# Kernel tuning notes

Measured on AMD Instinct MI355X. Metric: run time of the kernel, lower is better.

## Reference

```python
import jax, jax.numpy as jnp
import numpy as np
from jax import lax

B, K, D = 8, 256, 256
T_FRAMES = 2048
NH, HD = 4, 64          # num_heads_upsampling = 2*num_heads, head_dim = in_dim // NH
FW = FC = 8             # filter_size_w / filter_size_c
SW, SC = 16, 2          # swish_block_units


def setup_inputs() -> dict:
    key = jax.random.key(0)
    ks = jax.random.split(key, 24)
    rn = lambda i, shape, s=0.05: jax.random.normal(ks[i], shape, jnp.float32) * s
    return {
        'phs': rn(0, (B, K, D), 1.0),
        'phs_mask': jnp.ones((B, K), bool),
        'total_duration_groundtruth': jnp.full((B,), T_FRAMES, jnp.int32),
        'T': T_FRAMES,
        'Wd': rn(1, (D, 1)), 'bd': jnp.zeros((1,), jnp.float32),
        'W1': rn(2, (D, D)), 'b1': jnp.zeros((D,), jnp.float32),
        'W2': rn(3, (D, D)), 'b2': jnp.zeros((D,), jnp.float32),
        'W3': rn(4, (D, D)), 'b3': jnp.zeros((D,), jnp.float32),
        'wconv_k': rn(5, (FW, D, 3)), 'wconv_b': jnp.zeros((FW,), jnp.float32),
        'wln_g': jnp.ones((FW,), jnp.float32), 'wln_b': jnp.zeros((FW,), jnp.float32),
        'cconv_k': rn(6, (FC, D, 3)), 'cconv_b': jnp.zeros((FC,), jnp.float32),
        'cln_g': jnp.ones((FC,), jnp.float32), 'cln_b': jnp.zeros((FC,), jnp.float32),
        'sw1_W': rn(7, (FW + 2, SW)), 'sw1_b': jnp.zeros((SW,), jnp.float32),
        'sw2_W': rn(8, (SW, SW)), 'sw2_b': jnp.zeros((SW,), jnp.float32),
        'sc1_W': rn(9, (FC + 2, SC)), 'sc1_b': jnp.zeros((SC,), jnp.float32),
        'sc2_W': rn(10, (SC, SC)), 'sc2_b': jnp.zeros((SC,), jnp.float32),
        'we_W': rn(11, (SW, NH)), 'we_b': jnp.zeros((NH,), jnp.float32),
        'ce_W': rn(12, (SC, HD)), 'ce_b': jnp.zeros((HD,), jnp.float32),
    }


def _silu(x):
    return x * jax.nn.sigmoid(x)


def _conv_ln_silu(x, kern, bias, g, beta):
    # x: (b,k,D) -> Conv1d (same pad) -> LayerNorm over channel dim -> SiLU -> (b,k,F)
    y = lax.conv_general_dilated(x.transpose(0, 2, 1), kern, (1,), [(1, 1)],
                                 dimension_numbers=('NCH', 'OIH', 'NCH'))
    y = y + bias[None, :, None]
    mu = y.mean(1, keepdims=True)
    var = y.var(1, keepdims=True)
    y = (y - mu) * lax.rsqrt(var + 1e-5) * g[None, :, None] + beta[None, :, None]
    return _silu(y).transpose(0, 2, 1)


def _forward(phs, phs_mask, total_duration_groundtruth, t,
             Wd, bd, W1, b1, W2, b2, W3, b3,
             wconv_k, wconv_b, wln_g, wln_b, cconv_k, cconv_b, cln_g, cln_b,
             sw1_W, sw1_b, sw2_W, sw2_b, sc1_W, sc1_b, sc2_W, sc2_b,
             we_W, we_b, ce_W, ce_b):
    b, k, D = phs.shape
    nh, hd = NH, HD
    v_pad = ~phs_mask                                       # (b,k)
    # duration predictor (encoder substituted by identity; see notes)
    d_log = jax.nn.relu(phs @ Wd + bd)[..., 0]              # (b,k)
    d = jnp.clip(jnp.exp(d_log) - 1.0, 1e-12)
    d = jnp.where(v_pad, 0.0, d)
    d_pad = jnp.arange(t)[None, :] >= total_duration_groundtruth[:, None]  # (b,t)
    attn_mask = v_pad[:, None, :] | d_pad[:, :, None]       # (b,t,k)
    e = jnp.cumsum(d, -1)
    s = e - d
    scale = jnp.arange(1, t + 1, dtype=phs.dtype)[None, :, None]
    s_b = jnp.where(attn_mask, 0.0, scale - s[:, None, :])  # (b,t,k)
    e_b = jnp.where(attn_mask, 0.0, e[:, None, :] - scale)
    v = phs @ W1 + b1                                        # mha_project_1
    # w path: conv features broadcast over t + per-position MLP -> softmax scores
    w_convs = _conv_ln_silu(v, wconv_k, wconv_b, wln_g, wln_b)  # (b,k,FW)
    merged_w = jnp.concatenate([s_b[..., None], e_b[..., None],
                                jnp.broadcast_to(w_convs[:, None], (b, t, k, FW))], -1)
    hw = _silu(merged_w @ sw1_W + sw1_b)
    hw = _silu(hw @ sw2_W + sw2_b)                           # (b,t,k,SW)
    logits = (hw @ we_W + we_b).transpose(0, 3, 1, 2)        # (b,nh,t,k)
    logits = jnp.where(v_pad[:, None, None, :], -jnp.inf, logits)
    attn = jax.nn.softmax(logits, -1)                        # (b,nh,t,k)
    # c path
    c_convs = _conv_ln_silu(v, cconv_k, cconv_b, cln_g, cln_b)  # (b,k,FC)
    merged_c = jnp.concatenate([s_b[..., None], e_b[..., None],
                                jnp.broadcast_to(c_convs[:, None], (b, t, k, FC))], -1)
    hc = _silu(merged_c @ sc1_W + sc1_b)
    hc = _silu(hc @ sc2_W + sc2_b)                           # (b,t,k,SC)
    ein = jnp.einsum('bhtk,btkp->bhtp', attn, hc)            # (b,nh,t,SC)
    c_extra = (ein @ ce_W + ce_b).transpose(0, 2, 1, 3)      # (b,t,nh,hd)
    v4 = v.reshape(b, k, nh, hd).transpose(0, 2, 1, 3)       # (b,nh,k,hd)
    o_left = jnp.einsum('bhtk,bhkd->bhtd', attn, v4).transpose(0, 2, 1, 3)
    o_left = o_left.reshape(b, t, nh * hd) @ W2 + b2
    o_right = c_extra.reshape(b, t, nh * hd) @ W3 + b3
    out = o_left + o_right
    return out, d, attn


def reference(phs, phs_mask, total_duration_groundtruth, T,
              Wd, bd, W1, b1, W2, b2, W3, b3,
              wconv_k, wconv_b, wln_g, wln_b, cconv_k, cconv_b, cln_g, cln_b,
              sw1_W, sw1_b, sw2_W, sw2_b, sc1_W, sc1_b, sc2_W, sc2_b,
              we_W, we_b, ce_W, ce_b):
    return _forward(phs, phs_mask, total_duration_groundtruth, int(T),
                    Wd, bd, W1, b1, W2, b2, W3, b3,
                    wconv_k, wconv_b, wln_g, wln_b, cconv_k, cconv_b, cln_g, cln_b,
                    sw1_W, sw1_b, sw2_W, sw2_b, sc1_W, sc1_b, sc2_W, sc2_b,
                    we_W, we_b, ce_W, ce_b)
```

## Files before the change

kernel.cpp:

```cpp
#include <hip/hip_runtime.h>
#include <hip/hip_bf16.h>
#include <math.h>

#define BB 8
#define KK 256
#define DD 256
#define TT 2048
#define NH 4
#define HD 64
#define FW 8
#define FC 8
#define TPB 8
#define NK3 1088

#define OFF_S    0
#define OFF_E    (OFF_S + BB*KK)
#define OFF_V    (OFF_E + BB*KK)
#define OFF_WC   (OFF_V + BB*KK*DD)
#define OFF_CC   (OFF_WC + BB*KK*FW)
#define OFF_C0   (OFF_CC + BB*KK*FC)
#define OFF_W1T  (OFF_C0 + DD)
#define OFF_W2T  (OFF_W1T + DD*DD)
#define OFF_U2B  (OFF_W2T + DD*DD)
#define OFF_EINB (OFF_U2B + BB*DD*NK3/2)
#define OFF_P3   (OFF_EINB + BB*TT*64/2)

#define OUT_OUT  0
#define OUT_D    (BB*TT*DD)
#define OUT_ATTN (OUT_D + BB*KK)

typedef __attribute__((ext_vector_type(8))) short s8v;
typedef __attribute__((ext_vector_type(4))) float f4v;
typedef __attribute__((ext_vector_type(2))) _Float16 h2v;
typedef unsigned short ushort_t;

#define BC(x) __builtin_bit_cast(h2v, (unsigned int)(x))

__device__ __forceinline__ h2v pk(float a, float b) {
    return __builtin_bit_cast(h2v, __builtin_amdgcn_cvt_pkrtz(a, b));
}
__device__ __forceinline__ ushort_t f2bf(float x) {
    unsigned u = __float_as_uint(x);
    u += 0x7fffu + ((u >> 16) & 1u);
    return (ushort_t)(u >> 16);
}

#if __has_builtin(__builtin_amdgcn_fdot2)
#define FDOT2(a,b,c) __builtin_amdgcn_fdot2((a),(b),(c),false)
#else
__device__ __forceinline__ float FDOT2(h2v a, h2v b, float c) {
    return c + (float)a[0]*(float)b[0] + (float)a[1]*(float)b[1];
}
#endif

__device__ __forceinline__ float siluf(float z) {
    return z * __builtin_amdgcn_rcpf(1.0f + __expf(-z));
}

__device__ __forceinline__ float rsum64d(float x) {
    x += __int_as_float(__builtin_amdgcn_update_dpp(0, __float_as_int(x), 0x111, 0xf, 0xf, true));
    x += __int_as_float(__builtin_amdgcn_update_dpp(0, __float_as_int(x), 0x112, 0xf, 0xf, true));
    x += __int_as_float(__builtin_amdgcn_update_dpp(0, __float_as_int(x), 0x114, 0xf, 0xf, true));
    x += __int_as_float(__builtin_amdgcn_update_dpp(0, __float_as_int(x), 0x118, 0xf, 0xf, true));
    x += __int_as_float(__builtin_amdgcn_update_dpp(0, __float_as_int(x), 0x142, 0xa, 0xf, true));
    x += __int_as_float(__builtin_amdgcn_update_dpp(0, __float_as_int(x), 0x143, 0xc, 0xf, true));
    return x;
}
__device__ __forceinline__ float rmax64d(float x) {
    const int NI = 0xff800000;
    x = fmaxf(x, __int_as_float(__builtin_amdgcn_update_dpp(NI, __float_as_int(x), 0x111, 0xf, 0xf, false)));
    x = fmaxf(x, __int_as_float(__builtin_amdgcn_update_dpp(NI, __float_as_int(x), 0x112, 0xf, 0xf, false)));
    x = fmaxf(x, __int_as_float(__builtin_amdgcn_update_dpp(NI, __float_as_int(x), 0x114, 0xf, 0xf, false)));
    x = fmaxf(x, __int_as_float(__builtin_amdgcn_update_dpp(NI, __float_as_int(x), 0x118, 0xf, 0xf, false)));
    x = fmaxf(x, __int_as_float(__builtin_amdgcn_update_dpp(NI, __float_as_int(x), 0x142, 0xa, 0xf, false)));
    x = fmaxf(x, __int_as_float(__builtin_amdgcn_update_dpp(NI, __float_as_int(x), 0x143, 0xc, 0xf, false)));
    return x;
}
__device__ __forceinline__ float lane63f(float x) {
    return __int_as_float(__builtin_amdgcn_readlane(__float_as_int(x), 63));
}

__launch_bounds__(256)
__global__ void prep(const float* __restrict__ W1, const float* __restrict__ W2,
                     const float* __restrict__ phs, const float* __restrict__ Wd,
                     const float* __restrict__ bd,
                     const float* __restrict__ ceW, const float* __restrict__ ceb,
                     const float* __restrict__ W3, const float* __restrict__ b3,
                     const float* __restrict__ b2,
                     float* __restrict__ ws, float* __restrict__ dout) {
    __shared__ float tl[64][65];
    __shared__ float dbuf[KK];
    int role = blockIdx.x, tid = threadIdx.x;
    if (role < 32) {
        const float* src = (role < 16) ? W1 : W2;
        float* dst = ws + ((role < 16) ? OFF_W1T : OFF_W2T);
        int rr = role & 15;
        int r0 = (rr >> 2)*64, c0 = (rr & 3)*64;
        int rx = tid >> 4, col4 = (tid & 15)*4;
#pragma unroll
        for (int i = 0; i < 4; ++i) {
            int row = rx + i*16;
            float4 vld = *(const float4*)&src[(size_t)(r0+row)*256 + c0 + col4];
            tl[row][col4+0]=vld.x; tl[row][col4+1]=vld.y; tl[row][col4+2]=vld.z; tl[row][col4+3]=vld.w;
        }
        __syncthreads();
#pragma unroll
        for (int i = 0; i < 4; ++i) {
            int row = rx + i*16;
            float4 vst;
            vst.x = tl[col4+0][row]; vst.y = tl[col4+1][row];
            vst.z = tl[col4+2][row]; vst.w = tl[col4+3][row];
            *(float4*)&dst[(size_t)(c0+row)*256 + r0 + col4] = vst;
        }
    } else if (role < 40) {
        int b = role - 32;
        int wave = tid >> 6, lane = tid & 63;
        float4 w4 = ((const float4*)Wd)[lane];
        float bd0 = bd[0];
        for (int kk = 0; kk < 64; ++kk) {
            int k = wave*64 + kk;
            float4 p = ((const float4*)(phs + (size_t)(b*KK + k)*DD))[lane];
            float part = p.x*w4.x + p.y*w4.y + p.z*w4.z + p.w*w4.w;
            float tot = rsum64d(part);
            if (lane == 63) {
                float acc = tot + bd0;
                float dl = fmaxf(acc, 0.f);
                dbuf[k] = fmaxf(expf(dl) - 1.f, 1e-12f);
            }
        }
        __syncthreads();
        int k = tid;
        float dv = dbuf[k];
        for (int off = 1; off < KK; off <<= 1) {
            float t = (k >= off) ? dbuf[k-off] : 0.f;
            __syncthreads();
            dbuf[k] += t;
            __syncthreads();
        }
        float e = dbuf[k];
        dout[OUT_D + b*KK + k] = dv;
        ws[OFF_S + b*KK + k] = e - dv;
        ws[OFF_E + b*KK + k] = e;
    } else if (role < 48) {
        int b = role - 40, c = tid;
        float acc[8] = {0,0,0,0,0,0,0,0};
        float c0v = b3[c] + b2[c];
#pragma unroll 4
        for (int h = 0; h < NH; ++h) {
            for (int d = 0; d < HD; ++d) {
                float w3v = W3[(size_t)(h*HD + d)*DD + c];
                acc[h*2+0] = fmaf(ceW[d],      w3v, acc[h*2+0]);
                acc[h*2+1] = fmaf(ceW[HD + d], w3v, acc[h*2+1]);
                c0v        = fmaf(ceb[d],      w3v, c0v);
            }
        }
        ushort_t* rowp = (ushort_t*)(ws + OFF_U2B) + ((size_t)b*DD + c)*NK3 + 1024;
#pragma unroll
        for (int j = 0; j < 8; ++j) rowp[j] = f2bf(acc[j]);
#pragma unroll
        for (int j = 8; j < 64; ++j) rowp[j] = 0;
        if (b == 0) ws[OFF_C0 + c] = c0v;
    } else {
        uint4* ez = (uint4*)((ushort_t*)(ws + OFF_EINB));
        int base = (role - 48) * 2048 + tid;
#pragma unroll
        for (int i = 0; i < 8; ++i) {
            uint4 z; z.x = 0; z.y = 0; z.z = 0; z.w = 0;
            ez[base + i*256] = z;
        }
    }
}

__launch_bounds__(256)
__global__ void k3a(const float* __restrict__ vsrc, const float* __restrict__ wk,
                    const float* __restrict__ ck, float* __restrict__ part) {
    __shared__ float vt[KK][33];
    __shared__ float wl[32][3][8];
    int b = blockIdx.x, ch = blockIdx.y, ph = blockIdx.z;
    const float* kern = ph ? ck : wk;
    int tid = threadIdx.x, c0 = ch*32;
    for (int i = tid; i < 768; i += 256) {
        int f = i & 7;
        int cq = i >> 3; int q = cq % 3; int cc = cq / 3;
        wl[cc][q][f] = kern[(f*DD + c0 + cc)*3 + q];
    }
    {
        int cc = tid & 31, r8 = tid >> 5;
        for (int j = 0; j < 32; ++j) {
            int row = r8 + j*8;
            vt[row][cc] = vsrc[(size_t)(b*KK + row)*DD + c0 + cc];
        }
    }
    __syncthreads();
    int k = tid;
    float y[8] = {0.f,0.f,0.f,0.f,0.f,0.f,0.f,0.f};
    bool hm = (k > 0), hp = (k < KK-1);
    for (int cc = 0; cc < 32; ++cc) {
        float xm = hm ? vt[k-1][cc] : 0.f;
        float x0 = vt[k][cc];
        float xp = hp ? vt[k+1][cc] : 0.f;
        float4 a0 = *(const float4*)&wl[cc][0][0];
        float4 a1 = *(const float4*)&wl[cc][0][4];
        float4 b0 = *(const float4*)&wl[cc][1][0];
        float4 b1 = *(const float4*)&wl[cc][1][4];
        float4 c0v = *(const float4*)&wl[cc][2][0];
        float4 c1v = *(const float4*)&wl[cc][2][4];
        y[0] = fmaf(xm, a0.x, fmaf(x0, b0.x, fmaf(xp, c0v.x, y[0])));
        y[1] = fmaf(xm, a0.y, fmaf(x0, b0.y, fmaf(xp, c0v.y, y[1])));
        y[2] = fmaf(xm, a0.z, fmaf(x0, b0.z, fmaf(xp, c0v.z, y[2])));
        y[3] = fmaf(xm, a0.w, fmaf(x0, b0.w, fmaf(xp, c0v.w, y[3])));
        y[4] = fmaf(xm, a1.x, fmaf(x0, b1.x, fmaf(xp, c1v.x, y[4])));
        y[5] = fmaf(xm, a1.y, fmaf(x0, b1.y, fmaf(xp, c1v.y, y[5])));
        y[6] = fmaf(xm, a1.z, fmaf(x0, b1.z, fmaf(xp, c1v.z, y[6])));
        y[7] = fmaf(xm, a1.w, fmaf(x0, b1.w, fmaf(xp, c1v.w, y[7])));
    }
    float* pp = part + ((((size_t)(b*2 + ph))*8 + ch)*KK + k)*8;
    *(float4*)&pp[0] = make_float4(y[0],y[1],y[2],y[3]);
    *(float4*)&pp[4] = make_float4(y[4],y[5],y[6],y[7]);
}

__global__ void k3b(float* __restrict__ ws_, const float* __restrict__ part,
                    const float* __restrict__ wb, const float* __restrict__ wg, const float* __restrict__ wbe,
                    const float* __restrict__ cb, const float* __restrict__ cg, const float* __restrict__ cbe) {
    int b = blockIdx.x, k = threadIdx.x;
#pragma unroll
    for (int ph = 0; ph < 2; ++ph) {
        const float* bias = ph ? cb : wb;
        const float* g    = ph ? cg : wg;
        const float* beta = ph ? cbe : wbe;
        float y[8];
#pragma unroll
        for (int f = 0; f < 8; ++f) y[f] = bias[f];
        for (int ch = 0; ch < 8; ++ch) {
            const float* pp = part + ((((size_t)(b*2 + ph))*8 + ch)*KK + k)*8;
            float4 q0 = *(const float4*)&pp[0];
            float4 q1 = *(const float4*)&pp[4];
            y[0]+=q0.x; y[1]+=q0.y; y[2]+=q0.z; y[3]+=q0.w;
            y[4]+=q1.x; y[5]+=q1.y; y[6]+=q1.z; y[7]+=q1.w;
        }
        float mu = 0.f;
#pragma unroll
        for (int f = 0; f < 8; ++f) mu += y[f];
        mu *= 0.125f;
        float var = 0.f;
#pragma unroll
        for (int f = 0; f < 8; ++f) { float dd = y[f]-mu; var = fmaf(dd, dd, var); }
        var *= 0.125f;
        float inv = rsqrtf(var + 1e-5f);
        float* dst = ws_ + (ph ? OFF_CC : OFF_WC) + (size_t)(b*KK + k)*8;
#pragma unroll
        for (int f = 0; f < 8; ++f) {
            float z = (y[f]-mu)*inv*g[f] + beta[f];
            dst[f] = siluf(z);
        }
    }
}

__launch_bounds__(256, 3)
__global__ void k4_main(const float* __restrict__ ws, const int* __restrict__ tdur,
                        const float* __restrict__ sw1W, const float* __restrict__ sw1b,
                        const float* __restrict__ sw2W, const float* __restrict__ sw2b,
                        const float* __restrict__ weW, const float* __restrict__ web,
                        const float* __restrict__ sc1W, const float* __restrict__ sc1b,
                        const float* __restrict__ sc2W, const float* __restrict__ sc2b,
                        float* __restrict__ dout, ushort_t* __restrict__ einb) {
    __shared__ float sw1s[160];
    __shared__ float sw1bs[16];
    __shared__ float sc1s[20];
    __shared__ float sc1bs[2];
    __shared__ h2v   sw2h[16][8];
    __shared__ float sw2bias[16];
    __shared__ float wes4[16][4];
    __shared__ float webs[4], sc2s[4], sc2bs[2];
    __shared__ float red[4][4][16];
    __shared__ float gbuf[4][4][4];
    int tid = threadIdx.x;
    int b = blockIdx.y;
    int t0 = blockIdx.x * TPB;
    int lane = tid & 63, wid = tid >> 6;

    if (tid < 160) sw1s[tid] = sw1W[tid];
    if (tid < 16)  { sw1bs[tid] = sw1b[tid]; sw2bias[tid] = sw2b[tid]; }
    if (tid < 20)  sc1s[tid] = sc1W[tid];
    if (tid < 2)   { sc1bs[tid] = sc1b[tid]; sc2bs[tid] = sc2b[tid]; }
    if (tid < 4)   { webs[tid] = web[tid]; sc2s[tid] = sc2W[tid]; }
    if (tid < 128) {
        int j = tid >> 3, ip = tid & 7;
        sw2h[j][ip] = pk(sw2W[(2*ip)*16 + j], sw2W[(2*ip+1)*16 + j]);
    }
    if (tid < 64) wes4[tid>>2][tid&3] = weW[tid];
    __syncthreads();

    int k = tid;
    float s_k = ws[OFF_S + b*KK + k];
    float e_k = ws[OFF_E + b*KK + k];
    float al[16], be[16];
    float lgm[4], p2m[2];
    {
        float wcf[8];
        const float* wp = ws + OFF_WC + (size_t)(b*KK + k)*8;
#pragma unroll
        for (int f = 0; f < 8; ++f) wcf[f] = wp[f];
        float bw[16];
#pragma unroll
        for (int j = 0; j < 16; ++j) {
            float z = sw1bs[j];
#pragma unroll
            for (int f = 0; f < 8; ++f) z = fmaf(wcf[f], sw1s[(2+f)*16 + j], z);
            bw[j] = z;
        }
        h2v h1pm[8];
#pragma unroll
        for (int ip = 0; ip < 8; ++ip)
            h1pm[ip] = pk(siluf(bw[2*ip]), siluf(bw[2*ip+1]));
        lgm[0]=webs[0]; lgm[1]=webs[1]; lgm[2]=webs[2]; lgm[3]=webs[3];
#pragma unroll
        for (int j = 0; j < 16; ++j) {
            const uint4* wpq = (const uint4*)&sw2h[j][0];
            uint4 wa = wpq[0], wb = wpq[1];
            float z = sw2bias[j];
            z = FDOT2(h1pm[0], BC(wa.x), z); z = FDOT2(h1pm[1], BC(wa.y), z);
            z = FDOT2(h1pm[2], BC(wa.z), z); z = FDOT2(h1pm[3], BC(wa.w), z);
            z = FDOT2(h1pm[4], BC(wb.x), z); z = FDOT2(h1pm[5], BC(wb.y), z);
            z = FDOT2(h1pm[6], BC(wb.z), z); z = FDOT2(h1pm[7], BC(wb.w), z);
            float g = siluf(z);
            float4 wv = *(const float4*)&wes4[j][0];
            lgm[0] = fmaf(g, wv.x, lgm[0]); lgm[1] = fmaf(g, wv.y, lgm[1]);
            lgm[2] = fmaf(g, wv.z, lgm[2]); lgm[3] = fmaf(g, wv.w, lgm[3]);
        }
#pragma unroll
        for (int j = 0; j < 16; ++j) {
            float wsj = sw1s[j], wej = sw1s[16 + j];
            be[j] = wsj - wej;
            al[j] = bw[j] - wsj*s_k + wej*e_k;
        }
    }
    float gc[2], dc[2];
    {
        float ccf[8];
        const float* cp = ws + OFF_CC + (size_t)(b*KK + k)*8;
#pragma unroll
        for (int f = 0; f < 8; ++f) ccf[f] = cp[f];
        float bc0 = sc1bs[0], bc1 = sc1bs[1];
#pragma unroll
        for (int f = 0; f < 8; ++f) {
            bc0 = fmaf(ccf[f], sc1s[(2+f)*2 + 0], bc0);
            bc1 = fmaf(ccf[f], sc1s[(2+f)*2 + 1], bc1);
        }
        gc[0] = sc1s[0] - sc1s[2]; gc[1] = sc1s[1] - sc1s[3];
        dc[0] = bc0 - sc1s[0]*s_k + sc1s[2]*e_k;
        dc[1] = bc1 - sc1s[1]*s_k + sc1s[3]*e_k;
        float p1m0 = siluf(bc0), p1m1 = siluf(bc1);
        p2m[0] = siluf(p1m0*sc2s[0] + p1m1*sc2s[2] + sc2bs[0]);
        p2m[1] = siluf(p1m0*sc2s[1] + p1m1*sc2s[3] + sc2bs[1]);
    }
    float sc2r0 = sc2s[0], sc2r1 = sc2s[1], sc2r2 = sc2s[2], sc2r3 = sc2s[3];
    float sc2b0 = sc2bs[0], sc2b1 = sc2bs[1];
    float web0 = webs[0], web1 = webs[1], web2 = webs[2], web3 = webs[3];
    int td = tdur[b];

    for (int tg = 0; tg < TPB; tg += 4) {
        int tbase = t0 + tg;
        h2v h1p[4][8];
        float p2v[4][2];
        float lg[4][4];
        float ex[4][4];
#pragma unroll
        for (int u = 0; u < 4; ++u) {
            float tp1 = (float)(tbase + u + 1);
#pragma unroll
            for (int ip = 0; ip < 8; ++ip) {
                float z0 = siluf(fmaf(tp1, be[2*ip], al[2*ip]));
                float z1 = siluf(fmaf(tp1, be[2*ip+1], al[2*ip+1]));
                h1p[u][ip] = pk(z0, z1);
            }
            float p10 = siluf(fmaf(tp1, gc[0], dc[0]));
            float p11 = siluf(fmaf(tp1, gc[1], dc[1]));
            p2v[u][0] = siluf(p10*sc2r0 + p11*sc2r2 + sc2b0);
            p2v[u][1] = siluf(p10*sc2r1 + p11*sc2r3 + sc2b1);
            lg[u][0]=web0; lg[u][1]=web1; lg[u][2]=web2; lg[u][3]=web3;
        }
#pragma unroll
        for (int j = 0; j < 16; ++j) {
            const uint4* wpq = (const uint4*)&sw2h[j][0];
            uint4 wa = wpq[0], wb = wpq[1];
            h2v w0=BC(wa.x), w1=BC(wa.y), w2=BC(wa.z), w3=BC(wa.w);
            h2v w4_=BC(wb.x), w5=BC(wb.y), w6=BC(wb.z), w7=BC(wb.w);
            float bias = sw2bias[j];
            float4 wv = *(const float4*)&wes4[j][0];
#pragma unroll
            for (int u = 0; u < 4; ++u) {
                float z = bias;
                z = FDOT2(h1p[u][0], w0, z); z = FDOT2(h1p[u][1], w1, z);
                z = FDOT2(h1p[u][2], w2, z); z = FDOT2(h1p[u][3], w3, z);
                z = FDOT2(h1p[u][4], w4_, z); z = FDOT2(h1p[u][5], w5, z);
                z = FDOT2(h1p[u][6], w6, z); z = FDOT2(h1p[u][7], w7, z);
                float g = siluf(z);
                lg[u][0] = fmaf(g, wv.x, lg[u][0]);
                lg[u][1] = fmaf(g, wv.y, lg[u][1]);
                lg[u][2] = fmaf(g, wv.z, lg[u][2]);
                lg[u][3] = fmaf(g, wv.w, lg[u][3]);
            }
        }
#pragma unroll
        for (int u = 0; u < 4; ++u) {
            if ((tbase + u) >= td) {
                lg[u][0]=lgm[0]; lg[u][1]=lgm[1]; lg[u][2]=lgm[2]; lg[u][3]=lgm[3];
                p2v[u][0]=p2m[0]; p2v[u][1]=p2m[1];
            }
        }
#pragma unroll
        for (int u = 0; u < 4; ++u) {
            float m0 = lane63f(rmax64d(lg[u][0]));
            float m1 = lane63f(rmax64d(lg[u][1]));
            float m2 = lane63f(rmax64d(lg[u][2]));
            float m3 = lane63f(rmax64d(lg[u][3]));
            ex[u][0] = __expf(lg[u][0] - m0);
            ex[u][1] = __expf(lg[u][1] - m1);
            ex[u][2] = __expf(lg[u][2] - m2);
            ex[u][3] = __expf(lg[u][3] - m3);
            float s0 = rsum64d(ex[u][0]), s1 = rsum64d(ex[u][1]);
            float s2 = rsum64d(ex[u][2]), s3 = rsum64d(ex[u][3]);
            float u0 = rsum64d(ex[u][0]*p2v[u][0]);
            float u1 = rsum64d(ex[u][0]*p2v[u][1]);
            float u2 = rsum64d(ex[u][1]*p2v[u][0]);
            float u3 = rsum64d(ex[u][1]*p2v[u][1]);
            float u4 = rsum64d(ex[u][2]*p2v[u][0]);
            float u5 = rsum64d(ex[u][2]*p2v[u][1]);
            float u6 = rsum64d(ex[u][3]*p2v[u][0]);
            float u7 = rsum64d(ex[u][3]*p2v[u][1]);
            if (lane == 63) {
                float* rr = &red[u][wid][0];
                *(float4*)&rr[0]  = make_float4(m0, m1, m2, m3);
                *(float4*)&rr[4]  = make_float4(s0, s1, s2, s3);
                *(float4*)&rr[8]  = make_float4(u0, u1, u2, u3);
                *(float4*)&rr[12] = make_float4(u4, u5, u6, u7);
            }
        }
        __syncthreads();
        if (tid < 64) {
            int u = tid >> 4, h = (tid >> 2) & 3, w = tid & 3;
            float m0 = red[u][0][h], m1 = red[u][1][h], m2 = red[u][2][h], m3 = red[u][3][h];
            float M = fmaxf(fmaxf(m0, m1), fmaxf(m2, m3));
            float f0 = __expf(m0 - M), f1 = __expf(m1 - M);
            float f2 = __expf(m2 - M), f3 = __expf(m3 - M);
            float S = red[u][0][4+h]*f0 + red[u][1][4+h]*f1
                    + red[u][2][4+h]*f2 + red[u][3][4+h]*f3;
            float fw = (w == 0) ? f0 : ((w == 1) ? f1 : ((w == 2) ? f2 : f3));
            gbuf[u][w][h] = fw * __builtin_amdgcn_rcpf(S);
        } else if (tid < 96) {
            int idx = tid - 64, u = idx >> 3, j = idx & 7, h = j >> 1;
            float m0 = red[u][0][h], m1 = red[u][1][h], m2 = red[u][2][h], m3 = red[u][3][h];
            float M = fmaxf(fmaxf(m0, m1), fmaxf(m2, m3));
            float f0 = __expf(m0 - M), f1 = __expf(m1 - M);
            float f2 = __expf(m2 - M), f3 = __expf(m3 - M);
            float S = red[u][0][4+h]*f0 + red[u][1][4+h]*f1
                    + red[u][2][4+h]*f2 + red[u][3][4+h]*f3;
            float num = red[u][0][8+j]*f0 + red[u][1][8+j]*f1
                      + red[u][2][8+j]*f2 + red[u][3][8+j]*f3;
            einb[((size_t)b*TT + tbase + u)*64 + j] = f2bf(num * __builtin_amdgcn_rcpf(S));
        }
        __syncthreads();
#pragma unroll
        for (int u = 0; u < 4; ++u) {
            int t = tbase + u;
            float4 g4 = *(const float4*)&gbuf[u][wid][0];
            dout[OUT_ATTN + ((size_t)(b*NH + 0)*TT + t)*KK + k] = ex[u][0] * g4.x;
            dout[OUT_ATTN + ((size_t)(b*NH + 1)*TT + t)*KK + k] = ex[u][1] * g4.y;
            dout[OUT_ATTN + ((size_t)(b*NH + 2)*TT + t)*KK + k] = ex[u][2] * g4.z;
            dout[OUT_ATTN + ((size_t)(b*NH + 3)*TT + t)*KK + k] = ex[u][3] * g4.w;
        }
    }
}

#define MLDA 56
__launch_bounds__(256, 2)
__global__ void kmm(const float* __restrict__ A, const float* __restrict__ B,
                    float* __restrict__ C, const float* __restrict__ bias,
                    int Kd, int lda, int ldb, int ldc) {
    int m0 = blockIdx.x * 128, n0 = blockIdx.y * 128;
    __shared__ ushort_t Asl[128*MLDA];
    __shared__ ushort_t Bsl[128*MLDA];
    int tid = threadIdx.x;
    int lane = tid & 63, wid = tid >> 6;
    int wm = wid & 1, wn = wid >> 1;
    int quad = lane >> 4, lo = lane & 15;
    f4v acc[4][4];
#pragma unroll
    for (int i = 0; i < 4; ++i)
#pragma unroll
        for (int j = 0; j < 4; ++j) { f4v zz = {0.f,0.f,0.f,0.f}; acc[i][j] = zz; }
    int srow = tid >> 3;
    int scol = (tid & 7) * 4;
    for (int k0 = 0; k0 < Kd; k0 += 32) {
#pragma unroll
        for (int i = 0; i < 4; ++i) {
            int r = srow + i*32;
            float4 va = *(const float4*)&A[(size_t)(m0 + r)*lda + k0 + scol];
            float4 vb = *(const float4*)&B[(size_t)(n0 + r)*ldb + k0 + scol];
            __hip_bfloat162 pa0 = __float22bfloat162_rn(make_float2(va.x, va.y));
            __hip_bfloat162 pa1 = __float22bfloat162_rn(make_float2(va.z, va.w));
            __hip_bfloat162 pb0 = __float22bfloat162_rn(make_float2(vb.x, vb.y));
            __hip_bfloat162 pb1 = __float22bfloat162_rn(make_float2(vb.z, vb.w));
            *(uint2*)&Asl[r*MLDA + scol] = make_uint2(*(unsigned int*)&pa0, *(unsigned int*)&pa1);
            *(uint2*)&Bsl[r*MLDA + scol] = make_uint2(*(unsigned int*)&pb0, *(unsigned int*)&pb1);
        }
        __syncthreads();
        s8v af[4], bf[4];
#pragma unroll
        for (int mt = 0; mt < 4; ++mt)
            af[mt] = *(const s8v*)&Asl[(wm*64 + mt*16 + lo)*MLDA + quad*8];
#pragma unroll
        for (int nt = 0; nt < 4; ++nt)
            bf[nt] = *(const s8v*)&Bsl[(wn*64 + nt*16 + lo)*MLDA + quad*8];
#pragma unroll
        for (int mt = 0; mt < 4; ++mt)
#pragma unroll
            for (int nt = 0; nt < 4; ++nt)
                acc[mt][nt] = __builtin_amdgcn_mfma_f32_16x16x32_bf16(af[mt], bf[nt], acc[mt][nt], 0, 0, 0);
        __syncthreads();
    }
#pragma unroll
    for (int mt = 0; mt < 4; ++mt)
#pragma unroll
        for (int nt = 0; nt < 4; ++nt) {
            int col = n0 + wn*64 + nt*16 + lo;
            float bv = bias ? bias[col] : 0.f;
#pragma unroll
            for (int r = 0; r < 4; ++r) {
                int row = m0 + wm*64 + mt*16 + quad*4 + r;
                C[(size_t)row*ldc + col] = acc[mt][nt][r] + bv;
            }
        }
}

__launch_bounds__(256, 2)
__global__ void kmmB(const float* __restrict__ A, const float* __restrict__ B,
                     ushort_t* __restrict__ C,
                     int Kd, int lda, int ldb, int ldc,
                     long sA2, long sB1, long sB2, long sC1, long sC2, int nz2) {
    int z = blockIdx.z, z1 = z / nz2, z2 = z - z1*nz2;
    A += (size_t)z2*sA2;
    B += (size_t)z1*sB1 + (size_t)z2*sB2;
    C += (size_t)z1*sC1 + (size_t)z2*sC2;
    int m0 = blockIdx.x * 128, n0 = blockIdx.y * 128;
    __shared__ ushort_t Asl[128*MLDA];
    __shared__ ushort_t Bsl[128*MLDA];
    int tid = threadIdx.x;
    int lane = tid & 63, wid = tid >> 6;
    int wm = wid & 1, wn = wid >> 1;
    int quad = lane >> 4, lo = lane & 15;
    f4v acc[4][4];
#pragma unroll
    for (int i = 0; i < 4; ++i)
#pragma unroll
        for (int j = 0; j < 4; ++j) { f4v zz = {0.f,0.f,0.f,0.f}; acc[i][j] = zz; }
    int srow = tid >> 3;
    int scol = (tid & 7) * 4;
    for (int k0 = 0; k0 < Kd; k0 += 32) {
#pragma unroll
        for (int i = 0; i < 4; ++i) {
            int r = srow + i*32;
            float4 va = *(const float4*)&A[(size_t)(m0 + r)*lda + k0 + scol];
            float4 vb = *(const float4*)&B[(size_t)(n0 + r)*ldb + k0 + scol];
            __hip_bfloat162 pa0 = __float22bfloat162_rn(make_float2(va.x, va.y));
            __hip_bfloat162 pa1 = __float22bfloat162_rn(make_float2(va.z, va.w));
            __hip_bfloat162 pb0 = __float22bfloat162_rn(make_float2(vb.x, vb.y));
            __hip_bfloat162 pb1 = __float22bfloat162_rn(make_float2(vb.z, vb.w));
            *(uint2*)&Asl[r*MLDA + scol] = make_uint2(*(unsigned int*)&pa0, *(unsigned int*)&pa1);
            *(uint2*)&Bsl[r*MLDA + scol] = make_uint2(*(unsigned int*)&pb0, *(unsigned int*)&pb1);
        }
        __syncthreads();
        s8v af[4], bf[4];
#pragma unroll
        for (int mt = 0; mt < 4; ++mt)
            af[mt] = *(const s8v*)&Asl[(wm*64 + mt*16 + lo)*MLDA + quad*8];
#pragma unroll
        for (int nt = 0; nt < 4; ++nt)
            bf[nt] = *(const s8v*)&Bsl[(wn*64 + nt*16 + lo)*MLDA + quad*8];
#pragma unroll
        for (int mt = 0; mt < 4; ++mt)
#pragma unroll
            for (int nt = 0; nt < 4; ++nt)
                acc[mt][nt] = __builtin_amdgcn_mfma_f32_16x16x32_bf16(af[mt], bf[nt], acc[mt][nt], 0, 0, 0);
        __syncthreads();
    }
#pragma unroll
    for (int mt = 0; mt < 4; ++mt)
#pragma unroll
        for (int nt = 0; nt < 4; ++nt) {
            int col = n0 + wn*64 + nt*16 + lo;
#pragma unroll
            for (int r = 0; r < 4; ++r) {
                int row = m0 + wm*64 + mt*16 + quad*4 + r;
                C[(size_t)row*ldc + col] = f2bf(acc[mt][nt][r]);
            }
        }
}

#define OLD 72
__launch_bounds__(256, 4)
__global__ void kOL3(const float* __restrict__ attn, const ushort_t* __restrict__ einb,
                     const ushort_t* __restrict__ U2B, const float* __restrict__ C0,
                     float* __restrict__ out) {
    __shared__ ushort_t Asl[64*OLD];
    __shared__ ushort_t Bsl[128*OLD];
    int b = blockIdx.z;
    int t0 = blockIdx.x * 64, c0 = blockIdx.y * 128;
    int tid = threadIdx.x;
    int lane = tid & 63, wid = tid >> 6;
    int wm = wid & 1, wn = wid >> 1;
    int quad = lane >> 4, lo = lane & 15;
    f4v acc[2][4];
#pragma unroll
    for (int i = 0; i < 2; ++i)
#pragma unroll
        for (int j = 0; j < 4; ++j) { f4v zz = {0.f,0.f,0.f,0.f}; acc[i][j] = zz; }
    const float* Ab = attn + (size_t)b*NH*TT*KK;
    const ushort_t* Bb = U2B + (size_t)b*DD*NK3;
    int rA = tid >> 2, cA = (tid & 3) * 16;
    int rB = tid >> 1, cB = (tid & 1) * 32;
    for (int k0 = 0; k0 < NK3; k0 += 64) {
        if (k0 < NH*KK) {
            const float* ag = Ab + ((size_t)((k0 >> 8)*TT + t0 + rA))*KK + (k0 & 255) + cA;
#pragma unroll
            for (int i = 0; i < 4; ++i) {
                float4 va = *(const float4*)(ag + i*4);
                __hip_bfloat162 p0 = __float22bfloat162_rn(make_float2(va.x, va.y));
                __hip_bfloat162 p1 = __float22bfloat162_rn(make_float2(va.z, va.w));
                *(uint2*)&Asl[rA*OLD + cA + i*4] = make_uint2(*(unsigned int*)&p0, *(unsigned int*)&p1);
            }
        } else {
            const ushort_t* ag = einb + ((size_t)b*TT + t0 + rA)*64 + cA;
#pragma unroll
            for (int i = 0; i < 2; ++i)
                *(uint4*)&Asl[rA*OLD + cA + i*8] = *(const uint4*)(ag + i*8);
        }
        {
            const ushort_t* bg = Bb + (size_t)(c0 + rB)*NK3 + k0 + cB;
#pragma unroll
            for (int i = 0; i < 4; ++i)
                *(uint4*)&Bsl[rB*OLD + cB + i*8] = *(const uint4*)(bg + i*8);
        }
        __syncthreads();
        s8v af[2][2], bf[4][2];
#pragma unroll
        for (int mt = 0; mt < 2; ++mt)
#pragma unroll
            for (int ks = 0; ks < 2; ++ks)
                af[mt][ks] = *(const s8v*)&Asl[(wm*32 + mt*16 + lo)*OLD + ks*32 + quad*8];
#pragma unroll
        for (int nt = 0; nt < 4; ++nt)
#pragma unroll
            for (int ks = 0; ks < 2; ++ks)
                bf[nt][ks] = *(const s8v*)&Bsl[(wn*64 + nt*16 + lo)*OLD + ks*32 + quad*8];
#pragma unroll
        for (int mt = 0; mt < 2; ++mt)
#pragma unroll
            for (int nt = 0; nt < 4; ++nt)
#pragma unroll
                for (int ks = 0; ks < 2; ++ks)
                    acc[mt][nt] = __builtin_amdgcn_mfma_f32_16x16x32_bf16(af[mt][ks], bf[nt][ks], acc[mt][nt], 0, 0, 0);
        __syncthreads();
    }
#pragma unroll
    for (int mt = 0; mt < 2; ++mt)
#pragma unroll
        for (int nt = 0; nt < 4; ++nt) {
            int col = c0 + wn*64 + nt*16 + lo;
            float bv = C0[col];
#pragma unroll
            for (int r = 0; r < 4; ++r) {
                int row = t0 + wm*32 + mt*16 + quad*4 + r;
                out[((size_t)b*TT + row)*DD + col] = acc[mt][nt][r] + bv;
            }
        }
}

extern "C" void kernel_launch(void* const* d_in, const int* in_sizes, int n_in,
                              void* d_out, int out_size, void* d_ws, size_t ws_size,
                              hipStream_t stream) {
    const float* phs  = (const float*)d_in[0];
    const int*   tdur = (const int*)d_in[2];
    const float* Wd   = (const float*)d_in[4];
    const float* bd   = (const float*)d_in[5];
    const float* W1   = (const float*)d_in[6];
    const float* b1   = (const float*)d_in[7];
    const float* W2   = (const float*)d_in[8];
    const float* b2   = (const float*)d_in[9];
    const float* W3   = (const float*)d_in[10];
    const float* b3   = (const float*)d_in[11];
    const float* wck  = (const float*)d_in[12];
    const float* wcb  = (const float*)d_in[13];
    const float* wlg  = (const float*)d_in[14];
    const float* wlb  = (const float*)d_in[15];
    const float* cck  = (const float*)d_in[16];
    const float* ccb  = (const float*)d_in[17];
    const float* clg  = (const float*)d_in[18];
    const float* clb  = (const float*)d_in[19];
    const float* sw1W = (const float*)d_in[20];
    const float* sw1b = (const float*)d_in[21];
    const float* sw2W = (const float*)d_in[22];
    const float* sw2b = (const float*)d_in[23];
    const float* sc1W = (const float*)d_in[24];
    const float* sc1b = (const float*)d_in[25];
    const float* sc2W = (const float*)d_in[26];
    const float* sc2b = (const float*)d_in[27];
    const float* weW  = (const float*)d_in[28];
    const float* web  = (const float*)d_in[29];
    const float* ceW  = (const float*)d_in[30];
    const float* ceb  = (const float*)d_in[31];

    float* out = (float*)d_out;
    float* ws  = (float*)d_ws;
    ushort_t* U2B  = (ushort_t*)(ws + OFF_U2B);
    ushort_t* EINB = (ushort_t*)(ws + OFF_EINB);

    prep<<<112, 256, 0, stream>>>(W1, W2, phs, Wd, bd, ceW, ceb, W3, b3, b2, ws, out);
    kmm<<<dim3(16,2,1), 256, 0, stream>>>(phs, ws + OFF_W1T, ws + OFF_V, b1,
        256, 256, 256, 256);
    k3a<<<dim3(BB,8,2), 256, 0, stream>>>(ws + OFF_V, wck, cck, ws + OFF_P3);
    k3b<<<BB, 256, 0, stream>>>(ws, ws + OFF_P3, wcb, wlg, wlb, ccb, clg, clb);
    kmmB<<<dim3(2,2,32), 256, 0, stream>>>(ws + OFF_W2T, ws + OFF_V, U2B,
        64, 256, 256, NK3,
        64, (long)KK*DD, 64, (long)DD*NK3, 256, 4);
    k4_main<<<dim3(TT/TPB, BB), 256, 0, stream>>>(ws, tdur, sw1W, sw1b, sw2W, sw2b,
                                                  weW, web, sc1W, sc1b, sc2W, sc2b,
                                                  out, EINB);
    kOL3<<<dim3(TT/64, 2, BB), 256, 0, stream>>>(out + OUT_ATTN, EINB, U2B,
                                                 ws + OFF_C0, out);
}
```

Before: 366.6 us.

## Write bf16 attention copy in k4_main and fold k3b into kmmB launch

k4_main now writes a bf16 copy of the attention probabilities, plus the ein values, into a packed (t, NK3) bf16 buffer. kOL3 can then load its A operand as bf16 directly instead of reading fp32 attention and converting it. The conv LayerNorm/SiLU kernel k3b is merged into extra z-blocks of kmmB to save one launch. The cost is extra scattered 2-byte stores in k4_main and a larger workspace buffer.

```diff
diff --git a/kernel.cpp b/kernel.cpp
--- a/kernel.cpp
+++ b/kernel.cpp
@@ -22,8 +22,8 @@
 #define OFF_W1T  (OFF_C0 + DD)
 #define OFF_W2T  (OFF_W1T + DD*DD)
 #define OFF_U2B  (OFF_W2T + DD*DD)
-#define OFF_EINB (OFF_U2B + BB*DD*NK3/2)
-#define OFF_P3   (OFF_EINB + BB*TT*64/2)
+#define OFF_ATB  (OFF_U2B + BB*DD*NK3/2)
+#define OFF_P3   (OFF_ATB + BB*TT*NK3/2)
 
 #define OUT_OUT  0
 #define OUT_D    (BB*TT*DD)
@@ -161,13 +161,11 @@
         for (int j = 8; j < 64; ++j) rowp[j] = 0;
         if (b == 0) ws[OFF_C0 + c] = c0v;
     } else {
-        uint4* ez = (uint4*)((ushort_t*)(ws + OFF_EINB));
-        int base = (role - 48) * 2048 + tid;
-#pragma unroll
-        for (int i = 0; i < 8; ++i) {
-            uint4 z; z.x = 0; z.y = 0; z.z = 0; z.w = 0;
-            ez[base + i*256] = z;
-        }
+        int row = (role - 48) * 256 + tid;
+        ushort_t* rp = (ushort_t*)(ws + OFF_ATB) + (size_t)row*NK3 + 1024;
+        uint4 z; z.x = 0; z.y = 0; z.z = 0; z.w = 0;
+#pragma unroll
+        for (int i = 0; i < 8; ++i) *(uint4*)(rp + i*8) = z;
     }
 }
 
@@ -219,43 +217,6 @@
     *(float4*)&pp[4] = make_float4(y[4],y[5],y[6],y[7]);
 }
 
-__global__ void k3b(float* __restrict__ ws_, const float* __restrict__ part,
-                    const float* __restrict__ wb, const float* __restrict__ wg, const float* __restrict__ wbe,
-                    const float* __restrict__ cb, const float* __restrict__ cg, const float* __restrict__ cbe) {
-    int b = blockIdx.x, k = threadIdx.x;
-#pragma unroll
-    for (int ph = 0; ph < 2; ++ph) {
-        const float* bias = ph ? cb : wb;
-        const float* g    = ph ? cg : wg;
-        const float* beta = ph ? cbe : wbe;
-        float y[8];
-#pragma unroll
-        for (int f = 0; f < 8; ++f) y[f] = bias[f];
-        for (int ch = 0; ch < 8; ++ch) {
-            const float* pp = part + ((((size_t)(b*2 + ph))*8 + ch)*KK + k)*8;
-            float4 q0 = *(const float4*)&pp[0];
-            float4 q1 = *(const float4*)&pp[4];
-            y[0]+=q0.x; y[1]+=q0.y; y[2]+=q0.z; y[3]+=q0.w;
-            y[4]+=q1.x; y[5]+=q1.y; y[6]+=q1.z; y[7]+=q1.w;
-        }
-        float mu = 0.f;
-#pragma unroll
-        for (int f = 0; f < 8; ++f) mu += y[f];
-        mu *= 0.125f;
-        float var = 0.f;
-#pragma unroll
-        for (int f = 0; f < 8; ++f) { float dd = y[f]-mu; var = fmaf(dd, dd, var); }
-        var *= 0.125f;
-        float inv = rsqrtf(var + 1e-5f);
-        float* dst = ws_ + (ph ? OFF_CC : OFF_WC) + (size_t)(b*KK + k)*8;
-#pragma unroll
-        for (int f = 0; f < 8; ++f) {
-            float z = (y[f]-mu)*inv*g[f] + beta[f];
-            dst[f] = siluf(z);
-        }
-    }
-}
-
 __launch_bounds__(256, 3)
 __global__ void k4_main(const float* __restrict__ ws, const int* __restrict__ tdur,
                         const float* __restrict__ sw1W, const float* __restrict__ sw1b,
@@ -263,7 +224,7 @@
                         const float* __restrict__ weW, const float* __restrict__ web,
                         const float* __restrict__ sc1W, const float* __restrict__ sc1b,
                         const float* __restrict__ sc2W, const float* __restrict__ sc2b,
-                        float* __restrict__ dout, ushort_t* __restrict__ einb) {
+                        float* __restrict__ dout, ushort_t* __restrict__ atb) {
     __shared__ float sw1s[160];
     __shared__ float sw1bs[16];
     __shared__ float sc1s[20];
@@ -458,17 +419,24 @@
                     + red[u][2][4+h]*f2 + red[u][3][4+h]*f3;
             float num = red[u][0][8+j]*f0 + red[u][1][8+j]*f1
                       + red[u][2][8+j]*f2 + red[u][3][8+j]*f3;
-            einb[((size_t)b*TT + tbase + u)*64 + j] = f2bf(num * __builtin_amdgcn_rcpf(S));
+            atb[((size_t)b*TT + tbase + u)*NK3 + 1024 + j] = f2bf(num * __builtin_amdgcn_rcpf(S));
         }
         __syncthreads();
 #pragma unroll
         for (int u = 0; u < 4; ++u) {
             int t = tbase + u;
             float4 g4 = *(const float4*)&gbuf[u][wid][0];
-            dout[OUT_ATTN + ((size_t)(b*NH + 0)*TT + t)*KK + k] = ex[u][0] * g4.x;
-            dout[OUT_ATTN + ((size_t)(b*NH + 1)*TT + t)*KK + k] = ex[u][1] * g4.y;
-            dout[OUT_ATTN + ((size_t)(b*NH + 2)*TT + t)*KK + k] = ex[u][2] * g4.z;
-            dout[OUT_ATTN + ((size_t)(b*NH + 3)*TT + t)*KK + k] = ex[u][3] * g4.w;
+            float a0 = ex[u][0] * g4.x, a1 = ex[u][1] * g4.y;
+            float a2 = ex[u][2] * g4.z, a3 = ex[u][3] * g4.w;
+            dout[OUT_ATTN + ((size_t)(b*NH + 0)*TT + t)*KK + k] = a0;
+            dout[OUT_ATTN + ((size_t)(b*NH + 1)*TT + t)*KK + k] = a1;
+            dout[OUT_ATTN + ((size_t)(b*NH + 2)*TT + t)*KK + k] = a2;
+            dout[OUT_ATTN + ((size_t)(b*NH + 3)*TT + t)*KK + k] = a3;
+            ushort_t* ap = atb + ((size_t)b*TT + t)*NK3 + k;
+            ap[0]   = f2bf(a0);
+            ap[256] = f2bf(a1);
+            ap[512] = f2bf(a2);
+            ap[768] = f2bf(a3);
         }
     }
 }
@@ -538,7 +506,48 @@
 __global__ void kmmB(const float* __restrict__ A, const float* __restrict__ B,
                      ushort_t* __restrict__ C,
                      int Kd, int lda, int ldb, int ldc,
-                     long sA2, long sB1, long sB2, long sC1, long sC2, int nz2) {
+                     long sA2, long sB1, long sB2, long sC1, long sC2, int nz2,
+                     float* __restrict__ ws_, const float* __restrict__ part,
+                     const float* __restrict__ wb, const float* __restrict__ wg,
+                     const float* __restrict__ wbe,
+                     const float* __restrict__ cb, const float* __restrict__ cg,
+                     const float* __restrict__ cbe) {
+    if (blockIdx.z >= 32) {
+        if (blockIdx.x != 0 || blockIdx.y != 0) return;
+        int b = blockIdx.z - 32, k = threadIdx.x;
+#pragma unroll
+        for (int ph = 0; ph < 2; ++ph) {
+            const float* bias = ph ? cb : wb;
+            const float* g    = ph ? cg : wg;
+            const float* beta = ph ? cbe : wbe;
+            float y[8];
+#pragma unroll
+            for (int f = 0; f < 8; ++f) y[f] = bias[f];
+            for (int ch = 0; ch < 8; ++ch) {
+                const float* pp = part + ((((size_t)(b*2 + ph))*8 + ch)*KK + k)*8;
+                float4 q0 = *(const float4*)&pp[0];
+                float4 q1 = *(const float4*)&pp[4];
+                y[0]+=q0.x; y[1]+=q0.y; y[2]+=q0.z; y[3]+=q0.w;
+                y[4]+=q1.x; y[5]+=q1.y; y[6]+=q1.z; y[7]+=q1.w;
+            }
+            float mu = 0.f;
+#pragma unroll
+            for (int f = 0; f < 8; ++f) mu += y[f];
+            mu *= 0.125f;
+            float var = 0.f;
+#pragma unroll
+            for (int f = 0; f < 8; ++f) { float dd = y[f]-mu; var = fmaf(dd, dd, var); }
+            var *= 0.125f;
+            float inv = rsqrtf(var + 1e-5f);
+            float* dst = ws_ + (ph ? OFF_CC : OFF_WC) + (size_t)(b*KK + k)*8;
+#pragma unroll
+            for (int f = 0; f < 8; ++f) {
+                float z = (y[f]-mu)*inv*g[f] + beta[f];
+                dst[f] = siluf(z);
+            }
+        }
+        return;
+    }
     int z = blockIdx.z, z1 = z / nz2, z2 = z - z1*nz2;
     A += (size_t)z2*sA2;
     B += (size_t)z1*sB1 + (size_t)z2*sB2;
@@ -600,7 +609,7 @@
 
 #define OLD 72
 __launch_bounds__(256, 4)
-__global__ void kOL3(const float* __restrict__ attn, const ushort_t* __restrict__ einb,
+__global__ void kOL3(const ushort_t* __restrict__ atb,
                      const ushort_t* __restrict__ U2B, const float* __restrict__ C0,
                      float* __restrict__ out) {
     __shared__ ushort_t Asl[64*OLD];
@@ -616,25 +625,15 @@
     for (int i = 0; i < 2; ++i)
 #pragma unroll
         for (int j = 0; j < 4; ++j) { f4v zz = {0.f,0.f,0.f,0.f}; acc[i][j] = zz; }
-    const float* Ab = attn + (size_t)b*NH*TT*KK;
+    const ushort_t* Ab = atb + (size_t)b*TT*NK3;
     const ushort_t* Bb = U2B + (size_t)b*DD*NK3;
     int rA = tid >> 2, cA = (tid & 3) * 16;
     int rB = tid >> 1, cB = (tid & 1) * 32;
     for (int k0 = 0; k0 < NK3; k0 += 64) {
-        if (k0 < NH*KK) {
-            const float* ag = Ab + ((size_t)((k0 >> 8)*TT + t0 + rA))*KK + (k0 & 255) + cA;
-#pragma unroll
-            for (int i = 0; i < 4; ++i) {
-                float4 va = *(const float4*)(ag + i*4);
-                __hip_bfloat162 p0 = __float22bfloat162_rn(make_float2(va.x, va.y));
-                __hip_bfloat162 p1 = __float22bfloat162_rn(make_float2(va.z, va.w));
-                *(uint2*)&Asl[rA*OLD + cA + i*4] = make_uint2(*(unsigned int*)&p0, *(unsigned int*)&p1);
-            }
-        } else {
-            const ushort_t* ag = einb + ((size_t)b*TT + t0 + rA)*64 + cA;
-#pragma unroll
-            for (int i = 0; i < 2; ++i)
-                *(uint4*)&Asl[rA*OLD + cA + i*8] = *(const uint4*)(ag + i*8);
+        {
+            const ushort_t* ag = Ab + (size_t)(t0 + rA)*NK3 + k0 + cA;
+            *(uint4*)&Asl[rA*OLD + cA]     = *(const uint4*)(ag);
+            *(uint4*)&Asl[rA*OLD + cA + 8] = *(const uint4*)(ag + 8);
         }
         {
             const ushort_t* bg = Bb + (size_t)(c0 + rB)*NK3 + k0 + cB;
@@ -713,20 +712,19 @@
 
     float* out = (float*)d_out;
     float* ws  = (float*)d_ws;
-    ushort_t* U2B  = (ushort_t*)(ws + OFF_U2B);
-    ushort_t* EINB = (ushort_t*)(ws + OFF_EINB);
+    ushort_t* U2B = (ushort_t*)(ws + OFF_U2B);
+    ushort_t* ATB = (ushort_t*)(ws + OFF_ATB);
 
     prep<<<112, 256, 0, stream>>>(W1, W2, phs, Wd, bd, ceW, ceb, W3, b3, b2, ws, out);
     kmm<<<dim3(16,2,1), 256, 0, stream>>>(phs, ws + OFF_W1T, ws + OFF_V, b1,
         256, 256, 256, 256);
     k3a<<<dim3(BB,8,2), 256, 0, stream>>>(ws + OFF_V, wck, cck, ws + OFF_P3);
-    k3b<<<BB, 256, 0, stream>>>(ws, ws + OFF_P3, wcb, wlg, wlb, ccb, clg, clb);
-    kmmB<<<dim3(2,2,32), 256, 0, stream>>>(ws + OFF_W2T, ws + OFF_V, U2B,
+    kmmB<<<dim3(2,2,40), 256, 0, stream>>>(ws + OFF_W2T, ws + OFF_V, U2B,
         64, 256, 256, NK3,
-        64, (long)KK*DD, 64, (long)DD*NK3, 256, 4);
+        64, (long)KK*DD, 64, (long)DD*NK3, 256, 4,
+        ws, ws + OFF_P3, wcb, wlg, wlb, ccb, clg, clb);
     k4_main<<<dim3(TT/TPB, BB), 256, 0, stream>>>(ws, tdur, sw1W, sw1b, sw2W, sw2b,
                                                   weW, web, sc1W, sc1b, sc2W, sc2b,
-                                                  out, EINB);
-    kOL3<<<dim3(TT/64, 2, BB), 256, 0, stream>>>(out + OUT_ATTN, EINB, U2B,
-                                                 ws + OFF_C0, out);
-}
+                                                  out, ATB);
+    kOL3<<<dim3(TT/64, 2, BB), 256, 0, stream>>>(ATB, U2B, ws + OFF_C0, out);
+}
```

New measurement: 357.9 us. 1.02x faster.
